# Performance work log

Measured on AMD Instinct MI355X. Metric: run time of the kernel, lower is better.

Reference implementation:

```python
import jax, jax.numpy as jnp
import numpy as np

B, S, D, H = 2, 2048, 2048, 16
HD = D // H


def setup_inputs() -> dict:
    key = jax.random.key(0)
    ks = jax.random.split(key, 9)
    s = 1.0 / np.sqrt(D)
    return {
        "hidden_states": jax.random.normal(ks[0], (B, S, D), dtype=jnp.float32),
        "attention_mask": jnp.ones((B, 1, 1, S), dtype=jnp.int32),
        "Wq": jax.random.normal(ks[1], (D, D), dtype=jnp.float32) * s,
        "bq": jnp.zeros((D,), dtype=jnp.float32),
        "Wk": jax.random.normal(ks[2], (D, D), dtype=jnp.float32) * s,
        "bk": jnp.zeros((D,), dtype=jnp.float32),
        "Wv": jax.random.normal(ks[3], (D, D), dtype=jnp.float32) * s,
        "bv": jnp.zeros((D,), dtype=jnp.float32),
        "Wo": jax.random.normal(ks[4], (D, D), dtype=jnp.float32) * s,
        "bo": jnp.zeros((D,), dtype=jnp.float32),
    }


def reference(hidden_states, attention_mask, Wq, bq, Wk, bk, Wv, bv, Wo, bo):
    scale = 1.0 / np.sqrt(HD)
    # projections: torch Linear is x @ W.T + b
    q = hidden_states @ Wq.T + bq
    k = hidden_states @ Wk.T + bk
    v = hidden_states @ Wv.T + bv
    # [B,S,D] -> [B,H,S,hd]
    q = q.reshape(B, S, H, HD).transpose(0, 2, 1, 3)
    k = k.reshape(B, S, H, HD).transpose(0, 2, 1, 3)
    v = v.reshape(B, S, H, HD).transpose(0, 2, 1, 3)
    scores = jnp.einsum("bhqd,bhkd->bhqk", q, k) * scale
    scores = jnp.where(attention_mask == 0, jnp.float32(-1e9), scores)
    probs = jax.nn.softmax(scores, axis=-1)
    attn = jnp.einsum("bhqk,bhkd->bhqd", probs, v)
    attn = attn.transpose(0, 2, 1, 3).reshape(B, S, D)
    out = attn @ Wo.T + bo
    return out
```

## Files before the change

### kernel.cpp

```cpp
#include <hip/hip_runtime.h>
#include <hip/hip_bf16.h>
#include <stdint.h>

typedef __attribute__((ext_vector_type(8))) short short8;
typedef __attribute__((ext_vector_type(8))) unsigned short ushort8;
typedef __attribute__((ext_vector_type(4))) float f32x4;

#define DEVI __device__ __forceinline__

DEVI unsigned short f2bf(float f) {
    union { float f; unsigned int u; } a;
    a.f = f;
    unsigned int u = a.u;
    u += 0x7fffu + ((u >> 16) & 1u);
    return (unsigned short)(u >> 16);
}

DEVI void stage16(const unsigned short* g, unsigned short* ldsbase) {
    __builtin_amdgcn_global_load_lds(
        (const __attribute__((address_space(1))) void*)(uintptr_t)g,
        (__attribute__((address_space(3))) void*)(uintptr_t)ldsbase,
        16, 0, 0);
}

__global__ void cast_all(const float* __restrict__ hs, const float* __restrict__ wq,
                         const float* __restrict__ wk, const float* __restrict__ wv,
                         const float* __restrict__ wo, unsigned short* __restrict__ dst) {
    int i = blockIdx.x * blockDim.x + threadIdx.x;
    const float* src;
    int local;
    if (i < 1048576) { src = hs; local = i; }
    else {
        int j = i - 1048576;
        int w = j >> 19;
        local = j & 524287;
        src = (w == 0) ? wq : (w == 1) ? wk : (w == 2) ? wv : wo;
    }
    const float4* s = (const float4*)src;
    float4 x = s[2 * local], y = s[2 * local + 1];
    ushort8 o;
    o[0] = f2bf(x.x); o[1] = f2bf(x.y); o[2] = f2bf(x.z); o[3] = f2bf(x.w);
    o[4] = f2bf(y.x); o[5] = f2bf(y.y); o[6] = f2bf(y.z); o[7] = f2bf(y.w);
    *(ushort8*)(dst + 8 * i) = o;
}

template <int MODE>
__launch_bounds__(256, 2)
__global__ void gemm_nt(const unsigned short* __restrict__ A, const unsigned short* __restrict__ Bw,
                        const float* __restrict__ bias, void* __restrict__ Cout) {
    constexpr int K = 2048;
    __shared__ __align__(16) unsigned short As[128 * 32];
    __shared__ __align__(16) unsigned short Bs[128 * 32];
    const int tid = threadIdx.x;
    const int lane = tid & 63, wid = tid >> 6;
    const int quad = lane >> 4, l15 = lane & 15;
    const int m0 = blockIdx.y * 128, n0 = blockIdx.x * 128;
    const int wm = (wid & 1) * 64, wn = (wid >> 1) * 64;

    f32x4 acc[4][4];
#pragma unroll
    for (int i = 0; i < 4; i++)
#pragma unroll
        for (int j = 0; j < 4; j++) acc[i][j] = f32x4{0.f, 0.f, 0.f, 0.f};

    const int s0 = wid * 128 + lane, s1 = s0 + 64;
    const int r0 = s0 >> 2, c0 = (s0 & 3) ^ (r0 & 3);
    const int r1 = s1 >> 2, c1 = (s1 & 3) ^ (r1 & 3);
    unsigned short* ldsA0 = &As[(wid * 128) * 8];
    unsigned short* ldsA1 = &As[(wid * 128 + 64) * 8];
    unsigned short* ldsB0 = &Bs[(wid * 128) * 8];
    unsigned short* ldsB1 = &Bs[(wid * 128 + 64) * 8];
    const unsigned short* Ag0 = &A[(m0 + r0) * K + c0 * 8];
    const unsigned short* Ag1 = &A[(m0 + r1) * K + c1 * 8];
    const unsigned short* Bg0 = &Bw[(n0 + r0) * K + c0 * 8];
    const unsigned short* Bg1 = &Bw[(n0 + r1) * K + c1 * 8];

    for (int k0 = 0; k0 < K; k0 += 32) {
        __syncthreads();
        stage16(Ag0 + k0, ldsA0);
        stage16(Ag1 + k0, ldsA1);
        stage16(Bg0 + k0, ldsB0);
        stage16(Bg1 + k0, ldsB1);
        asm volatile("s_waitcnt vmcnt(0)" ::: "memory");
        __syncthreads();

        short8 af[4], bfr[4];
#pragma unroll
        for (int mi = 0; mi < 4; mi++) {
            int row = wm + mi * 16 + l15;
            int cc = quad ^ (row & 3);
            af[mi] = *(const short8*)&As[row * 32 + cc * 8];
        }
#pragma unroll
        for (int ni = 0; ni < 4; ni++) {
            int row = wn + ni * 16 + l15;
            int cc = quad ^ (row & 3);
            bfr[ni] = *(const short8*)&Bs[row * 32 + cc * 8];
        }
#pragma unroll
        for (int mi = 0; mi < 4; mi++)
#pragma unroll
            for (int ni = 0; ni < 4; ni++)
                acc[mi][ni] = __builtin_amdgcn_mfma_f32_16x16x32_bf16(af[mi], bfr[ni], acc[mi][ni], 0, 0, 0);
    }

#pragma unroll
    for (int mi = 0; mi < 4; mi++) {
#pragma unroll
        for (int ni = 0; ni < 4; ni++) {
            int n = n0 + wn + ni * 16 + l15;
            float bv = bias[n];
            if (MODE == 1) {
                int m_base = m0 + wm + mi * 16 + quad * 4;
                int h = n >> 7, dd = n & 127, bb = m_base >> 11, s = m_base & 2047;
                unsigned int v0 = f2bf(acc[mi][ni][0] + bv) | ((unsigned int)f2bf(acc[mi][ni][1] + bv) << 16);
                unsigned int v1 = f2bf(acc[mi][ni][2] + bv) | ((unsigned int)f2bf(acc[mi][ni][3] + bv) << 16);
                uint2 pk; pk.x = v0; pk.y = v1;
                *(uint2*)&((unsigned short*)Cout)[((bb * 16 + h) * 128 + dd) * 2048 + s] = pk;
            } else {
#pragma unroll
                for (int r = 0; r < 4; r++) {
                    int m = m0 + wm + mi * 16 + quad * 4 + r;
                    float val = acc[mi][ni][r] + bv;
                    if (MODE == 0) ((unsigned short*)Cout)[m * 2048 + n] = f2bf(val);
                    else           ((float*)Cout)[m * 2048 + n] = val;
                }
            }
        }
    }
}

__launch_bounds__(256, 2)
__global__ void attn_fused(const unsigned short* __restrict__ Q, const unsigned short* __restrict__ Kb,
                           const unsigned short* __restrict__ VT, const int* __restrict__ mask,
                           unsigned short* __restrict__ Ob) {
    __shared__ __align__(16) unsigned short Ks[64 * 128];
    __shared__ __align__(16) unsigned short Vs[128 * 64];
    __shared__ __align__(16) unsigned short Ps[4 * 32 * 72];
    const float C2 = 0.088388347648318447f * 1.4426950408889634f;

    const int tid = threadIdx.x;
    const int lane = tid & 63, wid = tid >> 6;
    const int quad = lane >> 4, l15 = lane & 15;
    const int qt = blockIdx.x, bh = blockIdx.y;
    const int b = bh >> 4, h = bh & 15;
    const int tok0 = b * 2048 + qt * 128 + wid * 32;

    short8 aq[2][4];
#pragma unroll
    for (int mi = 0; mi < 2; mi++)
#pragma unroll
        for (int c = 0; c < 4; c++)
            aq[mi][c] = *(const short8*)&Q[(tok0 + mi * 16 + l15) * 2048 + h * 128 + c * 32 + quad * 8];

    f32x4 oacc[2][8];
#pragma unroll
    for (int mi = 0; mi < 2; mi++)
#pragma unroll
        for (int c = 0; c < 8; c++) oacc[mi][c] = f32x4{0.f, 0.f, 0.f, 0.f};
    float lacc[2][4] = {{0.f, 0.f, 0.f, 0.f}, {0.f, 0.f, 0.f, 0.f}};

    const unsigned short* Kbase = Kb + b * 2048 * 2048 + h * 128;
    const unsigned short* Vbase = VT + (b * 16 + h) * 128 * 2048;

    const unsigned short* KgP[4];
    const unsigned short* VgP[4];
    unsigned short* ldsK[4];
    unsigned short* ldsV[4];
#pragma unroll
    for (int j = 0; j < 4; j++) {
        int s = wid * 256 + j * 64 + lane;
        int kr = s >> 4, kc = (s & 15) ^ (kr & 7);
        int vr = s >> 3, vc = (s & 7) ^ (vr & 7);
        KgP[j] = Kbase + kr * 2048 + kc * 8;
        VgP[j] = Vbase + vr * 2048 + vc * 8;
        ldsK[j] = &Ks[(wid * 256 + j * 64) * 8];
        ldsV[j] = &Vs[(wid * 256 + j * 64) * 8];
    }
    unsigned short* pw = &Ps[wid * 2304];

    for (int kt = 0; kt < 32; kt++) {
        const int key0 = kt * 64;
        __syncthreads();
#pragma unroll
        for (int j = 0; j < 4; j++) {
            stage16(KgP[j] + key0 * 2048, ldsK[j]);
            stage16(VgP[j] + key0, ldsV[j]);
        }
        int mk[4];
#pragma unroll
        for (int t = 0; t < 4; t++) mk[t] = mask[b * 2048 + key0 + t * 16 + l15];
        asm volatile("s_waitcnt vmcnt(0)" ::: "memory");
        __syncthreads();

        f32x4 sc[2][4];
#pragma unroll
        for (int mi = 0; mi < 2; mi++)
#pragma unroll
            for (int t = 0; t < 4; t++) sc[mi][t] = f32x4{0.f, 0.f, 0.f, 0.f};
#pragma unroll
        for (int c = 0; c < 4; c++)
#pragma unroll
            for (int t = 0; t < 4; t++) {
                int row = t * 16 + l15;
                int cc = (4 * c + quad) ^ (row & 7);
                short8 bk = *(const short8*)&Ks[row * 128 + cc * 8];
                sc[0][t] = __builtin_amdgcn_mfma_f32_16x16x32_bf16(aq[0][c], bk, sc[0][t], 0, 0, 0);
                sc[1][t] = __builtin_amdgcn_mfma_f32_16x16x32_bf16(aq[1][c], bk, sc[1][t], 0, 0, 0);
            }

#pragma unroll
        for (int mi = 0; mi < 2; mi++)
#pragma unroll
            for (int t = 0; t < 4; t++)
#pragma unroll
                for (int r = 0; r < 4; r++) {
                    float cs = mk[t] ? sc[mi][t][r] * C2 : -1e30f;
                    float p = __builtin_amdgcn_exp2f(cs);
                    lacc[mi][r] += p;
                    pw[(mi * 16 + quad * 4 + r) * 72 + t * 16 + l15] = f2bf(p);
                }
        asm volatile("s_waitcnt lgkmcnt(0)" ::: "memory");
        short8 ap[2][2];
#pragma unroll
        for (int mi = 0; mi < 2; mi++)
#pragma unroll
            for (int kk = 0; kk < 2; kk++)
                ap[mi][kk] = *(const short8*)&pw[(mi * 16 + l15) * 72 + kk * 32 + quad * 8];

#pragma unroll
        for (int kk = 0; kk < 2; kk++)
#pragma unroll
            for (int dt = 0; dt < 8; dt++) {
                int row = dt * 16 + l15;
                int cc = (kk * 4 + quad) ^ (row & 7);
                short8 bv = *(const short8*)&Vs[row * 64 + cc * 8];
                oacc[0][dt] = __builtin_amdgcn_mfma_f32_16x16x32_bf16(ap[0][kk], bv, oacc[0][dt], 0, 0, 0);
                oacc[1][dt] = __builtin_amdgcn_mfma_f32_16x16x32_bf16(ap[1][kk], bv, oacc[1][dt], 0, 0, 0);
            }
    }

    float inv[2][4];
#pragma unroll
    for (int mi = 0; mi < 2; mi++)
#pragma unroll
        for (int r = 0; r < 4; r++) {
            float l = lacc[mi][r];
#pragma unroll
            for (int off = 1; off < 16; off <<= 1) l += __shfl_xor(l, off, 64);
            inv[mi][r] = 1.0f / l;
        }
#pragma unroll
    for (int mi = 0; mi < 2; mi++)
#pragma unroll
        for (int dt = 0; dt < 8; dt++)
#pragma unroll
            for (int r = 0; r < 4; r++) {
                float val = oacc[mi][dt][r] * inv[mi][r];
                Ob[(tok0 + mi * 16 + quad * 4 + r) * 2048 + h * 128 + dt * 16 + l15] = f2bf(val);
            }
}

extern "C" void kernel_launch(void* const* d_in, const int* in_sizes, int n_in,
                              void* d_out, int out_size, void* d_ws, size_t ws_size,
                              hipStream_t stream) {
    const float* hs = (const float*)d_in[0];
    const int* mask = (const int*)d_in[1];
    const float* Wq = (const float*)d_in[2];
    const float* bq = (const float*)d_in[3];
    const float* Wk = (const float*)d_in[4];
    const float* bk = (const float*)d_in[5];
    const float* Wv = (const float*)d_in[6];
    const float* bv = (const float*)d_in[7];
    const float* Wo = (const float*)d_in[8];
    const float* bo = (const float*)d_in[9];

    unsigned short* hsb = (unsigned short*)d_ws;
    unsigned short* wqb = hsb + 8388608;
    unsigned short* wkb = wqb + 4194304;
    unsigned short* wvb = wkb + 4194304;
    unsigned short* wob = wvb + 4194304;
    unsigned short* qb  = wob + 4194304;
    unsigned short* kb  = qb  + 8388608;
    unsigned short* vtb = kb  + 8388608;
    unsigned short* ab  = vtb + 8388608;

    cast_all<<<12288, 256, 0, stream>>>(hs, Wq, Wk, Wv, Wo, hsb);

    gemm_nt<0><<<dim3(16, 32), 256, 0, stream>>>(hsb, wqb, bq, qb);
    gemm_nt<0><<<dim3(16, 32), 256, 0, stream>>>(hsb, wkb, bk, kb);
    gemm_nt<1><<<dim3(16, 32), 256, 0, stream>>>(hsb, wvb, bv, vtb);
    attn_fused<<<dim3(16, 32), 256, 0, stream>>>(qb, kb, vtb, mask, ab);
    gemm_nt<2><<<dim3(16, 32), 256, 0, stream>>>(ab, wob, bo, (float*)d_out);
}
```

Baseline: 426.3 us.

## Fuse QKV GEMMs, double-buffer LDS staging, fold softmax scale into Q

Merges the three Q/K/V projection GEMMs into one launch over a stacked weight matrix, using a 48x32 grid. Both GEMM kernels now double-buffer their LDS tiles so the next K-slice load overlaps the current MFMAs, which also halves the barriers per iteration. The attention scale and log2(e) factor are folded into Q at projection time, removing a multiply from the softmax inner loop, and launch bounds are raised to 3 blocks per SM for the QKV and attention kernels. The larger LDS footprint and the tighter register budget could limit occupancy or cause spills, and Q is rounded to bf16 after scaling, which slightly changes precision.

```diff
diff --git a/kernel.cpp b/kernel.cpp
--- a/kernel.cpp
+++ b/kernel.cpp
@@ -44,13 +44,109 @@
     *(ushort8*)(dst + 8 * i) = o;
 }
 
-template <int MODE>
+#define QSCALE 0.12751879523173862f
+
+__launch_bounds__(256, 3)
+__global__ void gemm_qkv(const unsigned short* __restrict__ A, const unsigned short* __restrict__ Bstack,
+                         const float* __restrict__ bq, const float* __restrict__ bk,
+                         const float* __restrict__ bv, unsigned short* __restrict__ qb,
+                         unsigned short* __restrict__ kb, unsigned short* __restrict__ vtb) {
+    constexpr int K = 2048;
+    __shared__ __align__(16) unsigned short As[2 * 4096];
+    __shared__ __align__(16) unsigned short Bs[2 * 4096];
+    const int tid = threadIdx.x;
+    const int lane = tid & 63, wid = tid >> 6;
+    const int quad = lane >> 4, l15 = lane & 15;
+    const int m0 = blockIdx.y * 128, n0 = blockIdx.x * 128;
+    const int mode = n0 >> 11;
+    const int wm = (wid & 1) * 64, wn = (wid >> 1) * 64;
+
+    f32x4 acc[4][4];
+#pragma unroll
+    for (int i = 0; i < 4; i++)
+#pragma unroll
+        for (int j = 0; j < 4; j++) acc[i][j] = f32x4{0.f, 0.f, 0.f, 0.f};
+
+    const int s0 = wid * 128 + lane, s1 = s0 + 64;
+    const int r0 = s0 >> 2, c0 = (s0 & 3) ^ (r0 & 3);
+    const int r1 = s1 >> 2, c1 = (s1 & 3) ^ (r1 & 3);
+    const int ldsoffA0 = wid * 1024, ldsoffA1 = wid * 1024 + 512;
+    const unsigned short* Ag0 = &A[(m0 + r0) * K + c0 * 8];
+    const unsigned short* Ag1 = &A[(m0 + r1) * K + c1 * 8];
+    const unsigned short* Bg0 = &Bstack[(n0 + r0) * K + c0 * 8];
+    const unsigned short* Bg1 = &Bstack[(n0 + r1) * K + c1 * 8];
+
+    stage16(Ag0, &As[ldsoffA0]);
+    stage16(Ag1, &As[ldsoffA1]);
+    stage16(Bg0, &Bs[ldsoffA0]);
+    stage16(Bg1, &Bs[ldsoffA1]);
+
+    for (int i = 0; i < 64; i++) {
+        const int cur = (i & 1) * 4096;
+        asm volatile("s_waitcnt vmcnt(0)" ::: "memory");
+        __syncthreads();
+        if (i < 63) {
+            const int nxt = 4096 - cur;
+            const int koff = (i + 1) * 32;
+            stage16(Ag0 + koff, &As[nxt + ldsoffA0]);
+            stage16(Ag1 + koff, &As[nxt + ldsoffA1]);
+            stage16(Bg0 + koff, &Bs[nxt + ldsoffA0]);
+            stage16(Bg1 + koff, &Bs[nxt + ldsoffA1]);
+        }
+        short8 af[4], bfr[4];
+#pragma unroll
+        for (int mi = 0; mi < 4; mi++) {
+            int row = wm + mi * 16 + l15;
+            int cc = quad ^ (row & 3);
+            af[mi] = *(const short8*)&As[cur + row * 32 + cc * 8];
+        }
+#pragma unroll
+        for (int ni = 0; ni < 4; ni++) {
+            int row = wn + ni * 16 + l15;
+            int cc = quad ^ (row & 3);
+            bfr[ni] = *(const short8*)&Bs[cur + row * 32 + cc * 8];
+        }
+#pragma unroll
+        for (int mi = 0; mi < 4; mi++)
+#pragma unroll
+            for (int ni = 0; ni < 4; ni++)
+                acc[mi][ni] = __builtin_amdgcn_mfma_f32_16x16x32_bf16(af[mi], bfr[ni], acc[mi][ni], 0, 0, 0);
+    }
+
+    const float* bias = (mode == 0) ? bq : (mode == 1) ? bk : bv;
+#pragma unroll
+    for (int mi = 0; mi < 4; mi++) {
+#pragma unroll
+        for (int ni = 0; ni < 4; ni++) {
+            int n = n0 + wn + ni * 16 + l15;
+            int nl = n & 2047;
+            float bb = bias[nl];
+            if (mode == 2) {
+                int m_base = m0 + wm + mi * 16 + quad * 4;
+                int h = nl >> 7, dd = nl & 127, bbb = m_base >> 11, s = m_base & 2047;
+                unsigned int v0 = f2bf(acc[mi][ni][0] + bb) | ((unsigned int)f2bf(acc[mi][ni][1] + bb) << 16);
+                unsigned int v1 = f2bf(acc[mi][ni][2] + bb) | ((unsigned int)f2bf(acc[mi][ni][3] + bb) << 16);
+                uint2 pk; pk.x = v0; pk.y = v1;
+                *(uint2*)&vtb[((bbb * 16 + h) * 128 + dd) * 2048 + s] = pk;
+            } else {
+                unsigned short* dst = (mode == 0) ? qb : kb;
+                float sc = (mode == 0) ? QSCALE : 1.0f;
+#pragma unroll
+                for (int r = 0; r < 4; r++) {
+                    int m = m0 + wm + mi * 16 + quad * 4 + r;
+                    dst[m * 2048 + nl] = f2bf((acc[mi][ni][r] + bb) * sc);
+                }
+            }
+        }
+    }
+}
+
 __launch_bounds__(256, 2)
-__global__ void gemm_nt(const unsigned short* __restrict__ A, const unsigned short* __restrict__ Bw,
-                        const float* __restrict__ bias, void* __restrict__ Cout) {
+__global__ void gemm_out(const unsigned short* __restrict__ A, const unsigned short* __restrict__ Bw,
+                         const float* __restrict__ bias, float* __restrict__ Cout) {
     constexpr int K = 2048;
-    __shared__ __align__(16) unsigned short As[128 * 32];
-    __shared__ __align__(16) unsigned short Bs[128 * 32];
+    __shared__ __align__(16) unsigned short As[2 * 4096];
+    __shared__ __align__(16) unsigned short Bs[2 * 4096];
     const int tid = threadIdx.x;
     const int lane = tid & 63, wid = tid >> 6;
     const int quad = lane >> 4, l15 = lane & 15;
@@ -66,36 +162,41 @@
     const int s0 = wid * 128 + lane, s1 = s0 + 64;
     const int r0 = s0 >> 2, c0 = (s0 & 3) ^ (r0 & 3);
     const int r1 = s1 >> 2, c1 = (s1 & 3) ^ (r1 & 3);
-    unsigned short* ldsA0 = &As[(wid * 128) * 8];
-    unsigned short* ldsA1 = &As[(wid * 128 + 64) * 8];
-    unsigned short* ldsB0 = &Bs[(wid * 128) * 8];
-    unsigned short* ldsB1 = &Bs[(wid * 128 + 64) * 8];
+    const int ldsoffA0 = wid * 1024, ldsoffA1 = wid * 1024 + 512;
     const unsigned short* Ag0 = &A[(m0 + r0) * K + c0 * 8];
     const unsigned short* Ag1 = &A[(m0 + r1) * K + c1 * 8];
     const unsigned short* Bg0 = &Bw[(n0 + r0) * K + c0 * 8];
     const unsigned short* Bg1 = &Bw[(n0 + r1) * K + c1 * 8];
 
-    for (int k0 = 0; k0 < K; k0 += 32) {
-        __syncthreads();
-        stage16(Ag0 + k0, ldsA0);
-        stage16(Ag1 + k0, ldsA1);
-        stage16(Bg0 + k0, ldsB0);
-        stage16(Bg1 + k0, ldsB1);
+    stage16(Ag0, &As[ldsoffA0]);
+    stage16(Ag1, &As[ldsoffA1]);
+    stage16(Bg0, &Bs[ldsoffA0]);
+    stage16(Bg1, &Bs[ldsoffA1]);
+
+    for (int i = 0; i < 64; i++) {
+        const int cur = (i & 1) * 4096;
         asm volatile("s_waitcnt vmcnt(0)" ::: "memory");
         __syncthreads();
-
+        if (i < 63) {
+            const int nxt = 4096 - cur;
+            const int koff = (i + 1) * 32;
+            stage16(Ag0 + koff, &As[nxt + ldsoffA0]);
+            stage16(Ag1 + koff, &As[nxt + ldsoffA1]);
+            stage16(Bg0 + koff, &Bs[nxt + ldsoffA0]);
+            stage16(Bg1 + koff, &Bs[nxt + ldsoffA1]);
+        }
         short8 af[4], bfr[4];
 #pragma unroll
         for (int mi = 0; mi < 4; mi++) {
             int row = wm + mi * 16 + l15;
             int cc = quad ^ (row & 3);
-            af[mi] = *(const short8*)&As[row * 32 + cc * 8];
+            af[mi] = *(const short8*)&As[cur + row * 32 + cc * 8];
         }
 #pragma unroll
         for (int ni = 0; ni < 4; ni++) {
             int row = wn + ni * 16 + l15;
             int cc = quad ^ (row & 3);
-            bfr[ni] = *(const short8*)&Bs[row * 32 + cc * 8];
+            bfr[ni] = *(const short8*)&Bs[cur + row * 32 + cc * 8];
         }
 #pragma unroll
         for (int mi = 0; mi < 4; mi++)
@@ -109,35 +210,23 @@
 #pragma unroll
         for (int ni = 0; ni < 4; ni++) {
             int n = n0 + wn + ni * 16 + l15;
-            float bv = bias[n];
-            if (MODE == 1) {
-                int m_base = m0 + wm + mi * 16 + quad * 4;
-                int h = n >> 7, dd = n & 127, bb = m_base >> 11, s = m_base & 2047;
-                unsigned int v0 = f2bf(acc[mi][ni][0] + bv) | ((unsigned int)f2bf(acc[mi][ni][1] + bv) << 16);
-                unsigned int v1 = f2bf(acc[mi][ni][2] + bv) | ((unsigned int)f2bf(acc[mi][ni][3] + bv) << 16);
-                uint2 pk; pk.x = v0; pk.y = v1;
-                *(uint2*)&((unsigned short*)Cout)[((bb * 16 + h) * 128 + dd) * 2048 + s] = pk;
-            } else {
-#pragma unroll
-                for (int r = 0; r < 4; r++) {
-                    int m = m0 + wm + mi * 16 + quad * 4 + r;
-                    float val = acc[mi][ni][r] + bv;
-                    if (MODE == 0) ((unsigned short*)Cout)[m * 2048 + n] = f2bf(val);
-                    else           ((float*)Cout)[m * 2048 + n] = val;
-                }
-            }
-        }
-    }
-}
-
-__launch_bounds__(256, 2)
+            float bb = bias[n];
+#pragma unroll
+            for (int r = 0; r < 4; r++) {
+                int m = m0 + wm + mi * 16 + quad * 4 + r;
+                Cout[m * 2048 + n] = acc[mi][ni][r] + bb;
+            }
+        }
+    }
+}
+
+__launch_bounds__(256, 3)
 __global__ void attn_fused(const unsigned short* __restrict__ Q, const unsigned short* __restrict__ Kb,
                            const unsigned short* __restrict__ VT, const int* __restrict__ mask,
                            unsigned short* __restrict__ Ob) {
     __shared__ __align__(16) unsigned short Ks[64 * 128];
     __shared__ __align__(16) unsigned short Vs[128 * 64];
     __shared__ __align__(16) unsigned short Ps[4 * 32 * 72];
-    const float C2 = 0.088388347648318447f * 1.4426950408889634f;
 
     const int tid = threadIdx.x;
     const int lane = tid & 63, wid = tid >> 6;
@@ -215,7 +304,7 @@
             for (int t = 0; t < 4; t++)
 #pragma unroll
                 for (int r = 0; r < 4; r++) {
-                    float cs = mk[t] ? sc[mi][t][r] * C2 : -1e30f;
+                    float cs = mk[t] ? sc[mi][t][r] : -1e30f;
                     float p = __builtin_amdgcn_exp2f(cs);
                     lacc[mi][r] += p;
                     pw[(mi * 16 + quad * 4 + r) * 72 + t * 16 + l15] = f2bf(p);
@@ -277,19 +366,19 @@
 
     unsigned short* hsb = (unsigned short*)d_ws;
     unsigned short* wqb = hsb + 8388608;
-    unsigned short* wkb = wqb + 4194304;
-    unsigned short* wvb = wkb + 4194304;
-    unsigned short* wob = wvb + 4194304;
+    unsigned short* wob = wqb + 3 * 4194304;
     unsigned short* qb  = wob + 4194304;
     unsigned short* kb  = qb  + 8388608;
     unsigned short* vtb = kb  + 8388608;
     unsigned short* ab  = vtb + 8388608;
 
+    unsigned short* wkb = wqb + 4194304;
+    unsigned short* wvb = wkb + 4194304;
+    (void)wkb; (void)wvb;
+
     cast_all<<<12288, 256, 0, stream>>>(hs, Wq, Wk, Wv, Wo, hsb);
 
-    gemm_nt<0><<<dim3(16, 32), 256, 0, stream>>>(hsb, wqb, bq, qb);
-    gemm_nt<0><<<dim3(16, 32), 256, 0, stream>>>(hsb, wkb, bk, kb);
-    gemm_nt<1><<<dim3(16, 32), 256, 0, stream>>>(hsb, wvb, bv, vtb);
+    gemm_qkv<<<dim3(48, 32), 256, 0, stream>>>(hsb, wqb, bq, bk, bv, qb, kb, vtb);
     attn_fused<<<dim3(16, 32), 256, 0, stream>>>(qb, kb, vtb, mask, ab);
-    gemm_nt<2><<<dim3(16, 32), 256, 0, stream>>>(ab, wob, bo, (float*)d_out);
-}
+    gemm_out<<<dim3(16, 32), 256, 0, stream>>>(ab, wob, bo, (float*)d_out);
+}
```

Measured after the change: 466.7 us. 9.5% more time.
